# Performance work log

Hardware: AMD Instinct MI355X
Metric: run time of the kernel (lower is better)

The kernel has to match this reference:

```python
import jax, jax.numpy as jnp
import numpy as np


def setup_inputs() -> dict:
    key = jax.random.key(0)
    n_class, n_support, n_query, feature_dim = 32, 16, 16, 1024
    n_rows = n_class * n_support + n_query * n_class  # 1024
    data = jax.random.normal(key, (n_rows, feature_dim), dtype=jnp.float32)
    return {"data": data, "n_class": n_class, "n_support": n_support, "n_query": n_query}


def reference(data, n_class, n_support, n_query):
    D = data.shape[-1]
    # support: [n_class, n_support, D]; query: [n_query*n_class, D]
    support = data[: n_class * n_support].reshape(n_class, n_support, D)
    query = data[n_class * n_support :]
    # attention score: tanh(elementwise product) summed over feature dim
    # scores: [Q, n_class, n_support]  (Q = n_query*n_class)
    scores = jnp.tanh(support[None, :, :, :] * query[:, None, None, :]).sum(-1)
    att = jax.nn.softmax(scores, axis=-1)  # softmax over n_support
    # weighted instance pooling -> prototypes per (query, class): [Q, n_class, D]
    proto = jnp.einsum("qcs,csd->qcd", att, support)
    return proto
```

## Files before the change

### kernel.cpp

```cpp
#include <hip/hip_runtime.h>
#include <stdint.h>

constexpr int NC = 32, NS = 16, NQ = 512, D = 1024;
constexpr int QPB = 16;
constexpr int NQW = 4;

typedef float v2f __attribute__((ext_vector_type(2)));
typedef float v4f __attribute__((ext_vector_type(4)));

__device__ __forceinline__ void quad_acc(v2f t01, v2f t23, float& acc) {
    v2f A, B;
    A.x = __builtin_amdgcn_exp2f(t01.x);
    A.y = __builtin_amdgcn_exp2f(t01.y);
    B.x = __builtin_amdgcn_exp2f(t23.x);
    B.y = __builtin_amdgcn_exp2f(t23.y);
    A += 1.f;
    B += 1.f;
    v2f prod = A * B;
    v2f sum  = A + B;
    acc = fmaf(sum.x, __builtin_amdgcn_rcpf(prod.x), acc);
    acc = fmaf(sum.y, __builtin_amdgcn_rcpf(prod.y), acc);
}

__device__ __forceinline__ void gload_lds16(const float* g, float* l) {
    __builtin_amdgcn_global_load_lds(
        (const __attribute__((address_space(1))) void*)g,
        (__attribute__((address_space(3))) void*)l,
        16, 0, 0);
}

__global__ __launch_bounds__(256, 2)
void proto_attn_kernel(const float* __restrict__ data, float* __restrict__ out) {
    const int c    = blockIdx.x;
    const int qt   = blockIdx.y;
    const int tid  = threadIdx.x;
    const int wave = tid >> 6;
    const int lane = tid & 63;

    __shared__ __align__(16) float buf[2][NS * 256];

    const float* sup = data + (size_t)c * NS * D;

    auto stage = [&](int p, int b) {
        #pragma unroll
        for (int r = 0; r < 4; ++r) {
            int row = 4 * wave + r;
            gload_lds16(sup + row * D + p * 256 + lane * 4,
                        &buf[b][row * 256]);
        }
    };

    const float K = 2.88539008177792681472f;
    const int q0 = qt * QPB + wave * NQW;
    const v4f* qg = reinterpret_cast<const v4f*>(data + (size_t)(NC * NS + q0) * D);

    stage(0, 0);
    __syncthreads();

    float sc[NQW][NS];
    #pragma unroll
    for (int r = 0; r < NQW; ++r)
        #pragma unroll
        for (int s = 0; s < NS; ++s) sc[r][s] = 0.f;

    #pragma unroll
    for (int p = 0; p < 4; ++p) {
        if (p < 3) stage(p + 1, (p + 1) & 1);
        v4f q[NQW];
        #pragma unroll
        for (int r = 0; r < NQW; ++r)
            q[r] = qg[r * 256 + (p << 6) + lane] * K;
        const v4f* B = reinterpret_cast<const v4f*>(buf[p & 1]);
        #pragma unroll
        for (int s = 0; s < NS; ++s) {
            v4f sv = B[(s << 6) + lane];
            #pragma unroll
            for (int r = 0; r < NQW; ++r)
                quad_acc(sv.xy * q[r].xy, sv.zw * q[r].zw, sc[r][s]);
        }
        if (p < 3) __syncthreads();
    }

    #pragma unroll
    for (int r = 0; r < NQW; ++r)
        #pragma unroll
        for (int s = 0; s < NS; ++s) {
            float v = sc[r][s];
            #pragma unroll
            for (int m = 32; m >= 1; m >>= 1) v += __shfl_xor(v, m, 64);
            sc[r][s] = (float)D - 2.f * v;
        }

    const float L2E = 1.44269504088896340736f;
    #pragma unroll
    for (int r = 0; r < NQW; ++r) {
        float mx = sc[r][0];
        #pragma unroll
        for (int s = 1; s < NS; ++s) mx = fmaxf(mx, sc[r][s]);
        float sum = 0.f;
        #pragma unroll
        for (int s = 0; s < NS; ++s) {
            sc[r][s] = __builtin_amdgcn_exp2f((sc[r][s] - mx) * L2E);
            sum += sc[r][s];
        }
        const float inv = __builtin_amdgcn_rcpf(sum);
        #pragma unroll
        for (int s = 0; s < NS; ++s) sc[r][s] *= inv;
    }

    auto proto_quarter = [&](int qq, int b) {
        const v4f* B = reinterpret_cast<const v4f*>(buf[b]);
        v2f oxy[NQW], ozw[NQW];
        #pragma unroll
        for (int r = 0; r < NQW; ++r) { oxy[r] = 0.f; ozw[r] = 0.f; }
        #pragma unroll
        for (int s = 0; s < NS; ++s) {
            v4f sv = B[(s << 6) + lane];
            #pragma unroll
            for (int r = 0; r < NQW; ++r) {
                oxy[r] += sv.xy * sc[r][s];
                ozw[r] += sv.zw * sc[r][s];
            }
        }
        #pragma unroll
        for (int r = 0; r < NQW; ++r) {
            v4f o; o.xy = oxy[r]; o.zw = ozw[r];
            v4f* og = reinterpret_cast<v4f*>(out + ((size_t)(q0 + r) * NC + c) * D);
            og[(qq << 6) + lane] = o;
        }
    };

    proto_quarter(2, 0);
    proto_quarter(3, 1);
    __syncthreads();
    stage(0, 0);
    stage(1, 1);
    __syncthreads();
    proto_quarter(0, 0);
    proto_quarter(1, 1);
}

extern "C" void kernel_launch(void* const* d_in, const int* in_sizes, int n_in,
                              void* d_out, int out_size, void* d_ws, size_t ws_size,
                              hipStream_t stream) {
    (void)in_sizes; (void)n_in; (void)out_size; (void)d_ws; (void)ws_size;
    const float* data = (const float*)d_in[0];
    float* out = (float*)d_out;
    dim3 grid(NC, NQ / QPB);
    proto_attn_kernel<<<grid, dim3(256), 0, stream>>>(data, out);
}
```

Measured before the change: 141.7 us.

## Split fused kernel into score and prototype kernels staging weights through output

The single fused kernel becomes two launches. The first computes the tanh scores and softmax and writes the 16 weights into the first elements of each output row. The second kernel reads those weights back and computes the weighted pooling, using 2 queries per wave and a larger grid, with double-buffered staging of the support rows. This is meant to cut register pressure in the pooling phase and to add parallelism there. In exchange it adds a second launch, reloads the support rows in both kernels, and relies on reading the weights before the same row is overwritten.

Measured after the change: 137.3 us. -3.1%, faster.

```diff
diff --git a/kernel.cpp b/kernel.cpp
--- a/kernel.cpp
+++ b/kernel.cpp
@@ -2,8 +2,6 @@
 #include <stdint.h>
 
 constexpr int NC = 32, NS = 16, NQ = 512, D = 1024;
-constexpr int QPB = 16;
-constexpr int NQW = 4;
 
 typedef float v2f __attribute__((ext_vector_type(2)));
 typedef float v4f __attribute__((ext_vector_type(4)));
@@ -30,7 +28,7 @@
 }
 
 __global__ __launch_bounds__(256, 2)
-void proto_attn_kernel(const float* __restrict__ data, float* __restrict__ out) {
+void score_kernel(const float* __restrict__ data, float* __restrict__ out) {
     const int c    = blockIdx.x;
     const int qt   = blockIdx.y;
     const int tid  = threadIdx.x;
@@ -38,51 +36,49 @@
     const int lane = tid & 63;
 
     __shared__ __align__(16) float buf[2][NS * 256];
-
     const float* sup = data + (size_t)c * NS * D;
 
     auto stage = [&](int p, int b) {
         #pragma unroll
         for (int r = 0; r < 4; ++r) {
             int row = 4 * wave + r;
-            gload_lds16(sup + row * D + p * 256 + lane * 4,
-                        &buf[b][row * 256]);
+            gload_lds16(sup + row * D + p * 256 + lane * 4, &buf[b][row * 256]);
         }
     };
 
     const float K = 2.88539008177792681472f;
-    const int q0 = qt * QPB + wave * NQW;
+    const int q0 = qt * 16 + wave * 4;
     const v4f* qg = reinterpret_cast<const v4f*>(data + (size_t)(NC * NS + q0) * D);
 
     stage(0, 0);
     __syncthreads();
 
-    float sc[NQW][NS];
+    float sc[4][NS];
     #pragma unroll
-    for (int r = 0; r < NQW; ++r)
+    for (int r = 0; r < 4; ++r)
         #pragma unroll
         for (int s = 0; s < NS; ++s) sc[r][s] = 0.f;
 
     #pragma unroll
     for (int p = 0; p < 4; ++p) {
         if (p < 3) stage(p + 1, (p + 1) & 1);
-        v4f q[NQW];
+        v4f q[4];
         #pragma unroll
-        for (int r = 0; r < NQW; ++r)
-            q[r] = qg[r * 256 + (p << 6) + lane] * K;
+        for (int r = 0; r < 4; ++r) q[r] = qg[r * 256 + (p << 6) + lane] * K;
         const v4f* B = reinterpret_cast<const v4f*>(buf[p & 1]);
         #pragma unroll
         for (int s = 0; s < NS; ++s) {
             v4f sv = B[(s << 6) + lane];
             #pragma unroll
-            for (int r = 0; r < NQW; ++r)
+            for (int r = 0; r < 4; ++r)
                 quad_acc(sv.xy * q[r].xy, sv.zw * q[r].zw, sc[r][s]);
         }
         if (p < 3) __syncthreads();
     }
 
+    const float L2E = 1.44269504088896340736f;
     #pragma unroll
-    for (int r = 0; r < NQW; ++r)
+    for (int r = 0; r < 4; ++r) {
         #pragma unroll
         for (int s = 0; s < NS; ++s) {
             float v = sc[r][s];
@@ -90,10 +86,6 @@
             for (int m = 32; m >= 1; m >>= 1) v += __shfl_xor(v, m, 64);
             sc[r][s] = (float)D - 2.f * v;
         }
-
-    const float L2E = 1.44269504088896340736f;
-    #pragma unroll
-    for (int r = 0; r < NQW; ++r) {
         float mx = sc[r][0];
         #pragma unroll
         for (int s = 1; s < NS; ++s) mx = fmaxf(mx, sc[r][s]);
@@ -108,36 +100,69 @@
         for (int s = 0; s < NS; ++s) sc[r][s] *= inv;
     }
 
-    auto proto_quarter = [&](int qq, int b) {
-        const v4f* B = reinterpret_cast<const v4f*>(buf[b]);
-        v2f oxy[NQW], ozw[NQW];
+    #pragma unroll
+    for (int r = 0; r < 4; ++r) {
+        float v = 0.f;
         #pragma unroll
-        for (int r = 0; r < NQW; ++r) { oxy[r] = 0.f; ozw[r] = 0.f; }
+        for (int s = 0; s < NS; ++s) v = (lane == s) ? sc[r][s] : v;
+        if (lane < NS)
+            out[((size_t)(q0 + r) * NC + c) * D + lane] = v;
+    }
+}
+
+__global__ __launch_bounds__(256, 2)
+void proto_kernel(const float* __restrict__ data, float* __restrict__ out) {
+    const int c    = blockIdx.x;
+    const int qt   = blockIdx.y;
+    const int tid  = threadIdx.x;
+    const int wave = tid >> 6;
+    const int lane = tid & 63;
+
+    __shared__ __align__(16) float buf[2][NS * 256];
+    const float* sup = data + (size_t)c * NS * D;
+
+    auto stage = [&](int p, int b) {
+        #pragma unroll
+        for (int r = 0; r < 4; ++r) {
+            int row = 4 * wave + r;
+            gload_lds16(sup + row * D + p * 256 + lane * 4, &buf[b][row * 256]);
+        }
+    };
+
+    const int q0 = qt * 8 + wave * 2;
+    float* orow0 = out + ((size_t)q0 * NC + c) * D;
+    float* orow1 = orow0 + (size_t)NC * D;
+
+    stage(0, 0);
+
+    float a0[NS], a1[NS];
+    #pragma unroll
+    for (int s = 0; s < NS; ++s) { a0[s] = orow0[s]; a1[s] = orow1[s]; }
+    __syncthreads();
+
+    v4f* og0 = reinterpret_cast<v4f*>(orow0);
+    v4f* og1 = reinterpret_cast<v4f*>(orow1);
+
+    #pragma unroll
+    for (int p = 0; p < 4; ++p) {
+        if (p < 3) stage(p + 1, (p + 1) & 1);
+        const v4f* B = reinterpret_cast<const v4f*>(buf[p & 1]);
+        v2f oxy0 = 0.f, ozw0 = 0.f, oxy1 = 0.f, ozw1 = 0.f;
         #pragma unroll
         for (int s = 0; s < NS; ++s) {
             v4f sv = B[(s << 6) + lane];
-            #pragma unroll
-            for (int r = 0; r < NQW; ++r) {
-                oxy[r] += sv.xy * sc[r][s];
-                ozw[r] += sv.zw * sc[r][s];
-            }
+            oxy0 += sv.xy * a0[s];
+            ozw0 += sv.zw * a0[s];
+            oxy1 += sv.xy * a1[s];
+            ozw1 += sv.zw * a1[s];
         }
-        #pragma unroll
-        for (int r = 0; r < NQW; ++r) {
-            v4f o; o.xy = oxy[r]; o.zw = ozw[r];
-            v4f* og = reinterpret_cast<v4f*>(out + ((size_t)(q0 + r) * NC + c) * D);
-            og[(qq << 6) + lane] = o;
-        }
-    };
-
-    proto_quarter(2, 0);
-    proto_quarter(3, 1);
-    __syncthreads();
-    stage(0, 0);
-    stage(1, 1);
-    __syncthreads();
-    proto_quarter(0, 0);
-    proto_quarter(1, 1);
+        v4f r0, r1;
+        r0.xy = oxy0; r0.zw = ozw0;
+        r1.xy = oxy1; r1.zw = ozw1;
+        og0[(p << 6) + lane] = r0;
+        og1[(p << 6) + lane] = r1;
+        if (p < 3) __syncthreads();
+    }
 }
 
 extern "C" void kernel_launch(void* const* d_in, const int* in_sizes, int n_in,
@@ -146,6 +171,6 @@
     (void)in_sizes; (void)n_in; (void)out_size; (void)d_ws; (void)ws_size;
     const float* data = (const float*)d_in[0];
     float* out = (float*)d_out;
-    dim3 grid(NC, NQ / QPB);
-    proto_attn_kernel<<<grid, dim3(256), 0, stream>>>(data, out);
+    score_kernel<<<dim3(NC, NQ / 16), dim3(256), 0, stream>>>(data, out);
+    proto_kernel<<<dim3(NC, NQ / 8), dim3(256), 0, stream>>>(data, out);
 }
```
